# Kernel tuning notes

Hardware: AMD Instinct MI355X
Metric: run time of the kernel (lower is better)

The kernel has to match this reference:

```python
import jax, jax.numpy as jnp
import numpy as np
from jax import lax

# Constants matching PostProcess(conf_thres=0.4, iou_thres=0.5, merge=False, agnostic=False)
CONF_THRES = 0.4
IOU_THRES = 0.5
MAX_WH = 4096.0   # per-class box offset (agnostic=False)
MAX_DET = 300     # hardcoded in module
MAX_NMS = 30000   # cap on NMS candidates (yolov5 convention); JAX needs static shapes
B, N, NC = 16, 25200, 80


def setup_inputs() -> dict:
    key = jax.random.key(0)
    u = jax.random.uniform(key, (B, N, 5 + NC), dtype=jnp.float32)
    # cx,cy in [0,640); w,h in [2,102); obj and class scores in [0,1)
    scale = jnp.concatenate([jnp.array([640.0, 640.0, 100.0, 100.0], jnp.float32),
                             jnp.ones((1 + NC,), jnp.float32)])
    shift = jnp.concatenate([jnp.array([0.0, 0.0, 2.0, 2.0], jnp.float32),
                             jnp.zeros((1 + NC,), jnp.float32)])
    prediction = u * scale + shift
    return {"prediction": prediction}


def _cxcywh_to_xyxy(x):
    cx, cy, w, h = x[..., 0], x[..., 1], x[..., 2], x[..., 3]
    return jnp.stack([cx - 0.5 * w, cy - 0.5 * h, cx + 0.5 * w, cy + 0.5 * h], axis=-1)


def _process_one(x):  # x: [N, 5+NC]
    obj = x[:, 4]
    cls_conf = x[:, 5:] * obj[:, None]          # x[:,5:] *= x[:,4:5]
    box = _cxcywh_to_xyxy(x[:, :4])             # [N, 4]
    # multi-label candidate mask: obj > conf AND class conf > conf (x[xc] then x[:,5:] > conf)
    cand = (obj[:, None] > CONF_THRES) & (cls_conf > CONF_THRES)   # [N, NC]
    flat = jnp.where(cand, cls_conf, 0.0).reshape(-1)              # [N*NC]
    top_scores, top_idx = lax.top_k(flat, MAX_NMS)                 # static-size candidate set
    bi = top_idx // NC                                             # box index i
    cj = (top_idx % NC).astype(jnp.float32)                        # class index j
    cand_boxes = box[bi]                                           # [M, 4]
    scores0 = jnp.where(top_scores > CONF_THRES, top_scores, 0.0)  # 0 marks invalid/suppressed
    off_boxes = cand_boxes + cj[:, None] * MAX_WH                  # per-class offset for NMS
    areas = (off_boxes[:, 2] - off_boxes[:, 0]) * (off_boxes[:, 3] - off_boxes[:, 1])
    idx_range = jnp.arange(MAX_NMS)

    def step(scores, _):
        # greedy NMS: pick best remaining, suppress IoU > thresh (torchvision semantics)
        idx = jnp.argmax(scores)
        s = scores[idx]
        keep = s > 0.0
        b = off_boxes[idx]
        lt = jnp.maximum(b[:2], off_boxes[:, :2])
        rb = jnp.minimum(b[2:], off_boxes[:, 2:])
        wh = jnp.clip(rb - lt, 0.0)
        inter = wh[:, 0] * wh[:, 1]
        iou = inter / (areas[idx] + areas - inter + 1e-9)
        suppress = (iou > IOU_THRES) | (idx_range == idx)
        return jnp.where(suppress, 0.0, scores), (idx, keep)

    _, (keep_idx, keep_flag) = lax.scan(step, scores0, None, length=MAX_DET)
    rows = jnp.concatenate([cand_boxes[keep_idx],
                            top_scores[keep_idx][:, None],
                            cj[keep_idx][:, None]], axis=1)        # [MAX_DET, 6] = xyxy, conf, cls
    return jnp.where(keep_flag[:, None], rows, 0.0)


def reference(prediction):
    # Padded fixed-shape analogue of torch.stack(output): [B, MAX_DET, 6], zero rows = no detection
    return jax.vmap(_process_one)(prediction)
```

## Files before the change

kernel.cpp:

```cpp
#include <hip/hip_runtime.h>
#include <stdint.h>

#define BATCH 16
#define NROW 25200
#define NCLS 80
#define ROWF 85
#define MAXDET 300
#define MAXNMS 30000u
#define NBIN 3072
#define BASEBITS 0x3EC00000u
#define CAP 32768u
#define BATCH_FLOATS 2142000

#define PREBIN 2048
#define NBUCK 1024
#define CANDCAP 131072u
#define KMAX 2048u
#define TOPK 2048u
#define K2CAP 4096u

#define SORTCAP 1024
#define CH_SZ 128

#define TILE_ROWS 80
#define TILE_FLOATS 6800
#define RPB 400
#define SUBT 5
#define SBLK 63

#define ROWS_PER_BLK 256
#define SBLK2 99

__device__ __forceinline__ bool iou_gt_half(float ax1, float ay1, float ax2, float ay2, float aa,
                                            float bx1, float by1, float bx2, float by2, float ba) {
    float ltx = fmaxf(ax1, bx1), lty = fmaxf(ay1, by1);
    float rbx = fminf(ax2, bx2), rby = fminf(ay2, by2);
    float wx = fmaxf(__fsub_rn(rbx, ltx), 0.0f);
    float wy = fmaxf(__fsub_rn(rby, lty), 0.0f);
    float inter = __fmul_rn(wx, wy);
    float den = __fadd_rn(__fsub_rn(__fadd_rn(aa, ba), inter), 1e-9f);
    float t = __fmul_rn(0.5f, den);
    if (!(inter > t)) return false;
    float tg = __fmul_rn(0.50000012f, den);
    if (inter >= tg) return true;
    return __fdiv_rn(inter, den) > 0.5f;
}

__device__ __forceinline__ unsigned bin_of_bits(unsigned bits) {
    unsigned v = (bits - BASEBITS) >> 12;
    if (v > (unsigned)(NBIN - 1)) v = NBIN - 1;
    return v;
}

__global__ __launch_bounds__(256) void k_stage(const float* __restrict__ pred,
                                               unsigned* __restrict__ hist2,
                                               unsigned* __restrict__ ccnt,
                                               unsigned long long* __restrict__ cand,
                                               unsigned* __restrict__ oflow,
                                               int staged) {
    if (!staged) return;
    __shared__ unsigned shist[NBUCK];
    __shared__ unsigned long long skey[KMAX];
    __shared__ unsigned s_cnt, s_n, s_base;
    int bx = blockIdx.x;
    int b = bx / SBLK2, blk = bx - b * SBLK2;
    int t = threadIdx.x, lane = t & 63, wv = t >> 6;
    for (int i = t; i < NBUCK; i += 256) shist[i] = 0u;
    if (t == 0) s_cnt = 0u;
    __syncthreads();
    const float* pb = pred + (size_t)b * BATCH_FLOATS;
    int r0 = blk * ROWS_PER_BLK + wv * 64;
    int rown = NROW - r0;
    if (rown > 0) {
        if (rown > 64) rown = 64;
        float obj = 0.0f;
        if (lane < rown) obj = pb[(size_t)(r0 + lane) * ROWF + 4];
        unsigned long long live = __ballot(obj > 0.4f);
        while (live) {
            int j = (int)__builtin_ctzll(live);
            live &= live - 1ULL;
            float o = __shfl(obj, j);
            const float* rp = pb + (size_t)(r0 + j) * ROWF;
            unsigned grow = (unsigned)(r0 + j);
            {
                float s = __fmul_rn(rp[5 + lane], o);
                if (s >= 0.75f) {
                    unsigned bits = __float_as_uint(s);
                    unsigned bin = bin_of_bits(bits);
                    atomicAdd(&shist[bin - PREBIN], 1u);
                    unsigned u = atomicAdd(&s_cnt, 1u);
                    unsigned flat = grow * (unsigned)NCLS + (unsigned)lane;
                    if (u < KMAX)
                        skey[u] = ((unsigned long long)bits << 32) |
                                  (unsigned long long)(0xFFFFFFFFu - flat);
                    else oflow[b] = 1u;
                }
            }
            if (lane < 16) {
                int c = 64 + lane;
                float s = __fmul_rn(rp[5 + c], o);
                if (s >= 0.75f) {
                    unsigned bits = __float_as_uint(s);
                    unsigned bin = bin_of_bits(bits);
                    atomicAdd(&shist[bin - PREBIN], 1u);
                    unsigned u = atomicAdd(&s_cnt, 1u);
                    unsigned flat = grow * (unsigned)NCLS + (unsigned)c;
                    if (u < KMAX)
                        skey[u] = ((unsigned long long)bits << 32) |
                                  (unsigned long long)(0xFFFFFFFFu - flat);
                    else oflow[b] = 1u;
                }
            }
        }
    }
    __syncthreads();
    unsigned* gh = hist2 + (size_t)b * NBUCK;
    for (int i = t; i < NBUCK; i += 256) {
        unsigned v = shist[i];
        if (v) atomicAdd(&gh[i], v);
    }
    if (t == 0) {
        unsigned n = s_cnt;
        if (n > KMAX) n = KMAX;
        unsigned base = atomicAdd(&ccnt[b], n);
        if (base + n > CANDCAP) oflow[b] = 1u;
        s_n = n; s_base = base;
    }
    __syncthreads();
    unsigned n = s_n, base = s_base;
    if (base + n <= CANDCAP) {
        unsigned long long* cd = cand + (size_t)b * CANDCAP + base;
        for (unsigned k = t; k < n; k += 256) cd[k] = skey[k];
    }
}

__global__ __launch_bounds__(1024) void k_prep(const unsigned* __restrict__ hist2,
                                               const unsigned* __restrict__ ccnt,
                                               const unsigned* __restrict__ oflow,
                                               const unsigned long long* __restrict__ cand,
                                               unsigned* __restrict__ suf2,
                                               unsigned long long* __restrict__ keys2,
                                               int* __restrict__ meta,
                                               int staged) {
    __shared__ unsigned sS[NBUCK];
    __shared__ unsigned scur[NBUCK];
    __shared__ int s_cut, s_need, s_tot, s_T, s_valid;
    __shared__ unsigned s_bad, s_E;
    int b = blockIdx.x, t = threadIdx.x;
    unsigned h = hist2[(size_t)b * NBUCK + t];
    sS[t] = h;
    if (t == 0) { s_cut = -1; s_T = -1; s_bad = 0u; s_need = 0; s_tot = 0; s_E = 0u; }
    __syncthreads();
    if (h > (unsigned)SORTCAP) atomicOr(&s_bad, 1u);
    for (int off = 1; off < NBUCK; off <<= 1) {
        unsigned v = (t + off < NBUCK) ? sS[t + off] : 0u;
        __syncthreads();
        sS[t] += v;
        __syncthreads();
    }
    unsigned Sv = sS[t];
    unsigned Sn = (t + 1 < NBUCK) ? sS[t + 1] : 0u;
    if (Sv >= MAXNMS && Sn < MAXNMS) {
        s_cut = PREBIN + t; s_need = (int)(MAXNMS - Sn); s_tot = (int)Sv;
    }
    if (Sv >= TOPK && Sn < TOPK) { s_T = PREBIN + t; s_E = Sv; }
    unsigned* g2 = suf2 + (size_t)b * (NBUCK + 1);
    g2[t] = Sv;
    if (t == 0) g2[NBUCK] = 0u;
    scur[t] = Sn;
    __syncthreads();
    if (t == 0) {
        int valid = (staged && s_cut >= 0 && s_T >= 0 && s_bad == 0u &&
                     oflow[b] == 0u && ccnt[b] <= CANDCAP) ? 1 : 0;
        s_valid = valid;
        meta[b * 8 + 0] = valid ? s_cut : 0;
        meta[b * 8 + 1] = valid ? s_need : 0;
        meta[b * 8 + 2] = valid ? s_tot : 0;
        meta[b * 8 + 3] = valid;
        meta[b * 8 + 4] = valid ? s_T : 0;
        meta[b * 8 + 5] = valid ? (int)s_E : 0;
    }
    __syncthreads();
    if (s_valid) {
        int T = s_T;
        unsigned ccb = ccnt[b];
        const unsigned long long* cd = cand + (size_t)b * CANDCAP;
        unsigned long long* k2 = keys2 + (size_t)b * K2CAP;
        for (unsigned k = t; k < ccb; k += 1024) {
            unsigned long long key = cd[k];
            unsigned v = bin_of_bits((unsigned)(key >> 32));
            if ((int)v >= T) {
                unsigned pos = atomicAdd(&scur[v - PREBIN], 1u);
                if (pos < K2CAP) k2[pos] = key;
            }
        }
    }
}

__global__ __launch_bounds__(256) void k_hist_fb(const float* __restrict__ pred,
                                                 unsigned* __restrict__ hist,
                                                 const int* __restrict__ meta) {
    int bx = blockIdx.x;
    int b = bx / SBLK, blk = bx - b * SBLK;
    if (meta[b * 8 + 3]) return;
    __shared__ __align__(16) float rows[TILE_FLOATS];
    __shared__ unsigned shist[NBIN];
    int t = threadIdx.x, lane = t & 63, wv = t >> 6;
    for (int i = t; i < NBIN; i += 256) shist[i] = 0u;
    const float* pbase = pred + (size_t)b * BATCH_FLOATS + (size_t)blk * RPB * ROWF;
    for (int st = 0; st < SUBT; ++st) {
        __syncthreads();
        const float4* src = (const float4*)(pbase + (size_t)st * TILE_ROWS * ROWF);
        float4* dst = (float4*)rows;
        for (int i = t; i < TILE_FLOATS / 4; i += 256) dst[i] = src[i];
        __syncthreads();
        for (int r = wv; r < TILE_ROWS; r += 4) {
            float obj = rows[r * ROWF + 4];
            if (!(obj > 0.4f)) continue;
            for (int half = 0; half < 2; ++half) {
                int c = lane + (half << 6);
                if (c < NCLS) {
                    float s = __fmul_rn(rows[r * ROWF + 5 + c], obj);
                    if (s > 0.4f) atomicAdd(&shist[bin_of_bits(__float_as_uint(s))], 1u);
                }
            }
        }
    }
    __syncthreads();
    unsigned* gh = hist + (size_t)b * NBIN;
    for (int i = t; i < NBIN; i += 256) {
        unsigned v = shist[i];
        if (v) atomicAdd(&gh[i], v);
    }
}

__global__ __launch_bounds__(256) void k_scan_fb(const unsigned* __restrict__ hist,
                                                 unsigned* __restrict__ suf,
                                                 int* __restrict__ meta) {
    int b = blockIdx.x, t = threadIdx.x;
    if (meta[b * 8 + 3]) return;
    __shared__ unsigned sh[NBIN];
    __shared__ unsigned sS[NBIN];
    __shared__ unsigned cs[256];
    __shared__ int s_cut, s_need, s_tot;
    const unsigned* gh = hist + (size_t)b * NBIN;
    for (int i = t; i < NBIN; i += 256) sh[i] = gh[i];
    if (t == 0) { s_cut = 0; s_need = 0x7FFFFFFF; s_tot = 0; }
    __syncthreads();
    const int CHUNK = NBIN / 256;
    int base = t * CHUNK;
    unsigned tot = 0;
    for (int i = 0; i < CHUNK; ++i) tot += sh[base + i];
    cs[t] = tot;
    __syncthreads();
    for (int off = 1; off < 256; off <<= 1) {
        unsigned v = (t + off < 256) ? cs[t + off] : 0u;
        __syncthreads();
        cs[t] += v;
        __syncthreads();
    }
    unsigned after = (t + 1 < 256) ? cs[t + 1] : 0u;
    for (int i = CHUNK - 1; i >= 0; --i) {
        after += sh[base + i];
        sS[base + i] = after;
    }
    __syncthreads();
    unsigned* gs = suf + (size_t)b * (NBIN + 1);
    for (int i = t; i < NBIN; i += 256) gs[i] = sS[i];
    if (t == 0) gs[NBIN] = 0u;
    for (int i = 0; i < CHUNK; ++i) {
        int v = base + i;
        unsigned Sv = sS[v];
        unsigned Sn = (v + 1 < NBIN) ? sS[v + 1] : 0u;
        if (Sv >= MAXNMS && Sn < MAXNMS) {
            s_cut = v; s_need = (int)(MAXNMS - Sn); s_tot = (int)Sv;
        }
    }
    __syncthreads();
    if (t == 0) {
        int cut = s_cut, needv = s_need, totv = s_tot;
        if (sS[0] < MAXNMS) { cut = 0; needv = 0x7FFFFFFF; totv = (int)sS[0]; }
        meta[b * 8 + 0] = cut;
        meta[b * 8 + 1] = needv;
        meta[b * 8 + 2] = totv;
    }
}

__global__ __launch_bounds__(256) void k_scatter_fb(const float* __restrict__ pred,
                                                    const unsigned* __restrict__ suf,
                                                    const int* __restrict__ meta,
                                                    unsigned* __restrict__ cursor,
                                                    unsigned long long* __restrict__ keys) {
    int bx = blockIdx.x;
    int b = bx / SBLK, blk = bx - b * SBLK;
    if (meta[b * 8 + 3]) return;
    __shared__ __align__(16) float rows[TILE_FLOATS];
    int t = threadIdx.x, lane = t & 63, wv = t >> 6;
    int cutbin = meta[b * 8 + 0];
    const float* pbase = pred + (size_t)b * BATCH_FLOATS + (size_t)blk * RPB * ROWF;
    unsigned rowbase0 = (unsigned)(blk * RPB);
    const unsigned* gs = suf + (size_t)b * (NBIN + 1);
    unsigned* cur = cursor + (size_t)b * NBIN;
    unsigned long long* kb = keys + (size_t)b * CAP;
    for (int st = 0; st < SUBT; ++st) {
        __syncthreads();
        const float4* src = (const float4*)(pbase + (size_t)st * TILE_ROWS * ROWF);
        float4* dst = (float4*)rows;
        for (int i = t; i < TILE_FLOATS / 4; i += 256) dst[i] = src[i];
        __syncthreads();
        for (int r = wv; r < TILE_ROWS; r += 4) {
            float obj = rows[r * ROWF + 4];
            if (!(obj > 0.4f)) continue;
            unsigned grow = rowbase0 + (unsigned)(st * TILE_ROWS + r);
            for (int half = 0; half < 2; ++half) {
                int c = lane + (half << 6);
                if (c < NCLS) {
                    float s = __fmul_rn(rows[r * ROWF + 5 + c], obj);
                    if (s > 0.4f) {
                        unsigned bits = __float_as_uint(s);
                        unsigned bin = bin_of_bits(bits);
                        if ((int)bin >= cutbin) {
                            unsigned pos = gs[bin + 1] + atomicAdd(&cur[bin], 1u);
                            if (pos < CAP) {
                                unsigned flat = grow * (unsigned)NCLS + (unsigned)c;
                                kb[pos] = ((unsigned long long)bits << 32) |
                                          (unsigned long long)(0xFFFFFFFFu - flat);
                            }
                        }
                    }
                }
            }
        }
    }
}

__global__ __launch_bounds__(1024) void k_nms(const float* __restrict__ pred,
                                              const unsigned* __restrict__ suf,
                                              const unsigned* __restrict__ suf2,
                                              const int* __restrict__ meta,
                                              const unsigned* __restrict__ ccnt,
                                              const unsigned long long* __restrict__ keys,
                                              const unsigned long long* __restrict__ keys2,
                                              const unsigned long long* __restrict__ cand,
                                              float* __restrict__ out) {
    __shared__ unsigned sgsL[NBUCK + 1];
    __shared__ unsigned long long ktmp[SORTCAP];
    __shared__ unsigned long long skeys[SORTCAP];
    __shared__ unsigned maskW[CH_SZ][5];
    __shared__ unsigned sup0w[4];
    __shared__ float cbox[CH_SZ][9];
    __shared__ float kept[MAXDET][5];
    __shared__ int klist[MAXDET];
    __shared__ int s_nk, s_localk;
    __shared__ unsigned s_gc;

    int b = blockIdx.x;
    int tid = threadIdx.x;
    int lane = tid & 63, wv = tid >> 6;

    int cutbin = meta[b * 8 + 0];
    int needv  = meta[b * 8 + 1];
    unsigned total = (unsigned)meta[b * 8 + 2];
    int valid  = meta[b * 8 + 3];
    int Tbin   = meta[b * 8 + 4];
    unsigned E = valid ? (unsigned)meta[b * 8 + 5] : 0u;
    if (!valid && total > CAP) total = CAP;
    const unsigned* gs = suf + (size_t)b * (NBIN + 1);
    const unsigned* g2 = suf2 + (size_t)b * (NBUCK + 1);
    const unsigned long long* kb = keys + (size_t)b * CAP;
    const unsigned long long* k2 = keys2 + (size_t)b * K2CAP;
    const unsigned long long* cd = cand + (size_t)b * CANDCAP;
    unsigned ccb = valid ? ccnt[b] : 0u;
    if (ccb > CANDCAP) ccb = CANDCAP;
    const float* pb = pred + (size_t)b * BATCH_FLOATS;
    float* ob = out + (size_t)b * MAXDET * 6;

    if (valid) for (int i = tid; i < NBUCK + 1; i += 1024) sgsL[i] = g2[i];
    if (tid == 0) s_nk = 0;
    __syncthreads();

#define GSV(v) (valid ? sgsL[(v) - PREBIN] : gs[(v)])

    unsigned limit;
    if (needv == 0x7FFFFFFF) limit = total;
    else limit = GSV(cutbin + 1) + (unsigned)needv;
    if (limit > total) limit = total;

    unsigned p = 0;
    while (p < limit) {
        if (s_nk >= MAXDET) break;

        int lo = cutbin, hi = NBIN - 1, vs = NBIN - 1;
        while (lo <= hi) { int mid = (lo + hi) >> 1;
            if (GSV(mid) <= p + (unsigned)SORTCAP) { vs = mid; hi = mid - 1; } else lo = mid + 1; }
        unsigned gEnd = GSV(vs);
        bool phaseA = (!valid) || (p < E);
        if (valid && phaseA && gEnd > E) gEnd = E;
        if (gEnd > total) gEnd = total;
        if (gEnd <= p) { gEnd = p + (unsigned)SORTCAP; if (gEnd > total) gEnd = total; }
        unsigned G = gEnd - p;

        if (phaseA) {
            const unsigned long long* src = valid ? k2 : kb;
            unsigned myLo = 0, myHi = 0;
            unsigned long long raw = 0ULL;
            if (tid < (int)G) {
                unsigned idx = p + (unsigned)tid;
                int l2 = cutbin, h2 = NBIN - 1, v = cutbin;
                while (l2 <= h2) { int mid = (l2 + h2) >> 1;
                    if (GSV(mid) > idx) { v = mid; l2 = mid + 1; } else h2 = mid - 1; }
                unsigned bstart = GSV(v + 1);
                unsigned bend = GSV(v);
                raw = src[idx];
                myLo = (bstart > p) ? (bstart - p) : 0u;
                myHi = bend - p; if (myHi > G) myHi = G;
                ktmp[tid] = raw;
            }
            __syncthreads();
            if (tid < (int)G) {
                unsigned rank = 0;
                for (unsigned u = myLo; u < myHi; ++u) rank += (ktmp[u] > raw) ? 1u : 0u;
                skeys[myLo + rank] = raw;
            }
            __syncthreads();
        } else {
            int l0 = cutbin, h0 = NBIN - 1, w1 = cutbin;
            while (l0 <= h0) { int mid = (l0 + h0) >> 1;
                if (GSV(mid) > p) { w1 = mid; l0 = mid + 1; } else h0 = mid - 1; }
            if (tid == 0) s_gc = 0u;
            __syncthreads();
            for (unsigned k = tid; k < ccb; k += 1024) {
                unsigned long long key = cd[k];
                unsigned v = bin_of_bits((unsigned)(key >> 32));
                if ((int)v >= vs && (int)v <= w1) {
                    unsigned u = atomicAdd(&s_gc, 1u);
                    if (u < (unsigned)SORTCAP) ktmp[u] = key;
                }
            }
            __syncthreads();
            unsigned Gc = s_gc; if (Gc > (unsigned)SORTCAP) Gc = (unsigned)SORTCAP;
            if (tid < (int)Gc) {
                unsigned long long key = ktmp[tid];
                unsigned v = bin_of_bits((unsigned)(key >> 32));
                unsigned bstart = GSV(v + 1);
                unsigned rank = 0;
                for (unsigned u = 0; u < Gc; ++u) {
                    unsigned long long kk = ktmp[u];
                    unsigned vu = bin_of_bits((unsigned)(kk >> 32));
                    rank += (vu == v && kk > key) ? 1u : 0u;
                }
                skeys[(bstart - p) + rank] = key;
            }
            __syncthreads();
        }

        unsigned consumable = limit - p; if (consumable > G) consumable = G;

        for (unsigned c0 = 0; c0 < consumable; c0 += CH_SZ) {
            int nk0 = s_nk;
            if (nk0 >= MAXDET) break;
            int CH = (int)((consumable - c0 < (unsigned)CH_SZ) ? (consumable - c0) : (unsigned)CH_SZ);

            if (tid < CH_SZ * 5) maskW[tid / 5][tid % 5] = 0u;
            if (tid >= CH_SZ * 5 && tid < CH_SZ * 5 + 4) sup0w[tid - CH_SZ * 5] = 0u;
            if (tid < CH) {
                unsigned long long kk = skeys[c0 + tid];
                unsigned flat = 0xFFFFFFFFu - (unsigned)kk;
                unsigned bi = flat / (unsigned)NCLS;
                unsigned cc = flat - bi * (unsigned)NCLS;
                const float* rp = pb + (size_t)bi * ROWF;
                float cx = rp[0], cy = rp[1], wd = rp[2], ht = rp[3];
                float hw = __fmul_rn(0.5f, wd), hh = __fmul_rn(0.5f, ht);
                float off = __fmul_rn((float)cc, 4096.0f);
                float x1 = __fsub_rn(cx, hw), y1 = __fsub_rn(cy, hh);
                float x2 = __fadd_rn(cx, hw), y2 = __fadd_rn(cy, hh);
                float ox1 = __fadd_rn(x1, off), oy1 = __fadd_rn(y1, off);
                float ox2 = __fadd_rn(x2, off), oy2 = __fadd_rn(y2, off);
                cbox[tid][0] = ox1; cbox[tid][1] = oy1;
                cbox[tid][2] = ox2; cbox[tid][3] = oy2;
                cbox[tid][4] = __fmul_rn(__fsub_rn(ox2, ox1), __fsub_rn(oy2, oy1));
            }
            __syncthreads();

            {
                int col = tid & (CH_SZ - 1);
                int part = tid >> 7;
                if (col < CH) {
                    float bx1 = cbox[col][0], by1 = cbox[col][1];
                    float bx2 = cbox[col][2], by2 = cbox[col][3], ba = cbox[col][4];
                    unsigned part16 = 0u;
                    int rbase = part << 4;
                    for (int k = 0; k < 16; ++k) {
                        int i2 = rbase + k;
                        if (i2 >= col || i2 >= CH) break;
                        if (iou_gt_half(cbox[i2][0], cbox[i2][1], cbox[i2][2], cbox[i2][3],
                                        cbox[i2][4], bx1, by1, bx2, by2, ba))
                            part16 |= (1u << k);
                    }
                    if (part16)
                        atomicOr(&maskW[col][part >> 1], part16 << ((part & 1) << 4));
                    bool f = false;
                    for (int k2 = part; k2 < nk0; k2 += 8) {
                        if (iou_gt_half(kept[k2][0], kept[k2][1], kept[k2][2], kept[k2][3],
                                        kept[k2][4], bx1, by1, bx2, by2, ba)) f = true;
                    }
                    if (f) atomicOr(&sup0w[col >> 5], 1u << (col & 31));
                }
            }
            __syncthreads();

            if (wv == 0) {
                unsigned keptw = 0u;
                int nkv = nk0, lk = 0;
                unsigned pre0 = (lane < 4 && CH > 0) ? maskW[0][lane] : 0u;
                unsigned pre1 = (lane < 4 && CH > 1) ? maskW[1][lane] : 0u;
                for (int j = 0; j < CH && nkv < MAXDET; ++j) {
                    unsigned colw = pre0;
                    pre0 = pre1;
                    pre1 = (lane < 4 && (j + 2) < CH) ? maskW[j + 2][lane] : 0u;
                    bool hit = (keptw & colw) != 0u;
                    bool sup = __any(hit);
                    if ((sup0w[j >> 5] >> (j & 31)) & 1u) sup = true;
                    if (!sup) {
                        if (lane == (j >> 5)) keptw |= 1u << (j & 31);
                        if (lane == 0) klist[lk] = j;
                        lk++; nkv++;
                    }
                }
                if (lane == 0) { s_localk = lk; s_nk = nkv; }
            }
            __syncthreads();

            int lk = s_localk;
            for (int t2 = tid; t2 < lk; t2 += 1024) {
                int i = klist[t2];
                int oidx = nk0 + t2;
                kept[oidx][0] = cbox[i][0]; kept[oidx][1] = cbox[i][1];
                kept[oidx][2] = cbox[i][2]; kept[oidx][3] = cbox[i][3];
                kept[oidx][4] = cbox[i][4];
                unsigned long long kk = skeys[c0 + i];
                unsigned bits = (unsigned)(kk >> 32);
                unsigned flat = 0xFFFFFFFFu - (unsigned)kk;
                unsigned bi = flat / (unsigned)NCLS;
                unsigned cc = flat - bi * (unsigned)NCLS;
                const float* rp = pb + (size_t)bi * ROWF;
                float cx = rp[0], cy = rp[1], wd = rp[2], ht = rp[3];
                float hw = __fmul_rn(0.5f, wd), hh = __fmul_rn(0.5f, ht);
                float* orow = ob + (size_t)oidx * 6;
                orow[0] = __fsub_rn(cx, hw);
                orow[1] = __fsub_rn(cy, hh);
                orow[2] = __fadd_rn(cx, hw);
                orow[3] = __fadd_rn(cy, hh);
                orow[4] = __uint_as_float(bits);
                orow[5] = (float)cc;
            }
            __syncthreads();
        }
        p = gEnd;
    }
#undef GSV
}

extern "C" void kernel_launch(void* const* d_in, const int* in_sizes, int n_in,
                              void* d_out, int out_size, void* d_ws, size_t ws_size,
                              hipStream_t stream) {
    const float* pred = (const float*)d_in[0];
    float* outp = (float*)d_out;
    char* ws = (char*)d_ws;

    const size_t OFF_HIST  = 0;
    const size_t SZ_HIST   = (size_t)BATCH * NBIN * 4;
    const size_t OFF_CUR   = OFF_HIST + SZ_HIST;
    const size_t SZ_CUR    = (size_t)BATCH * NBIN * 4;
    const size_t OFF_H2    = OFF_CUR + SZ_CUR;
    const size_t SZ_H2     = (size_t)BATCH * NBUCK * 4;
    const size_t OFF_CCNT  = OFF_H2 + SZ_H2;
    const size_t SZ_CCNT   = (size_t)BATCH * 4;
    const size_t OFF_OFLW  = OFF_CCNT + SZ_CCNT;
    const size_t SZ_OFLW   = (size_t)BATCH * 4;
    const size_t OFF_META  = OFF_OFLW + SZ_OFLW;
    const size_t SZ_META   = (size_t)BATCH * 8 * 4;
    const size_t ZERO_SZ   = OFF_META + SZ_META;
    const size_t OFF_SUF   = ZERO_SZ;
    const size_t SZ_SUF    = (size_t)BATCH * (NBIN + 1) * 4;
    const size_t OFF_SUF2  = OFF_SUF + SZ_SUF;
    const size_t SZ_SUF2   = (size_t)BATCH * (NBUCK + 1) * 4;
    const size_t OFF_KEYS  = OFF_SUF2 + SZ_SUF2;
    const size_t SZ_KEYS   = (size_t)BATCH * CAP * 8;
    const size_t OFF_K2    = OFF_KEYS + SZ_KEYS;
    const size_t SZ_K2     = (size_t)BATCH * K2CAP * 8;
    const size_t OFF_CAND  = OFF_K2 + SZ_K2;
    const size_t SZ_CAND   = (size_t)BATCH * CANDCAP * 8;
    const size_t WS_NEEDED = OFF_CAND + SZ_CAND;

    int staged = (ws_size >= WS_NEEDED) ? 1 : 0;

    unsigned* hist             = (unsigned*)(ws + OFF_HIST);
    unsigned* cursor           = (unsigned*)(ws + OFF_CUR);
    unsigned* hist2            = (unsigned*)(ws + OFF_H2);
    unsigned* ccnt             = (unsigned*)(ws + OFF_CCNT);
    unsigned* oflow            = (unsigned*)(ws + OFF_OFLW);
    int* meta                  = (int*)(ws + OFF_META);
    unsigned* suf              = (unsigned*)(ws + OFF_SUF);
    unsigned* suf2             = (unsigned*)(ws + OFF_SUF2);
    unsigned long long* keys   = (unsigned long long*)(ws + OFF_KEYS);
    unsigned long long* keys2  = (unsigned long long*)(ws + OFF_K2);
    unsigned long long* cand   = (unsigned long long*)(ws + OFF_CAND);

    hipMemsetAsync(ws, 0, ZERO_SZ, stream);
    hipMemsetAsync(d_out, 0, (size_t)out_size * sizeof(float), stream);

    k_stage<<<dim3(BATCH * SBLK2), dim3(256), 0, stream>>>(pred, hist2, ccnt, cand, oflow, staged);
    k_prep<<<dim3(BATCH), dim3(1024), 0, stream>>>(hist2, ccnt, oflow, cand, suf2, keys2, meta, staged);
    k_hist_fb<<<dim3(BATCH * SBLK), dim3(256), 0, stream>>>(pred, hist, meta);
    k_scan_fb<<<dim3(BATCH), dim3(256), 0, stream>>>(hist, suf, meta);
    k_scatter_fb<<<dim3(BATCH * SBLK), dim3(256), 0, stream>>>(pred, suf, meta, cursor, keys);
    k_nms<<<dim3(BATCH), dim3(1024), 0, stream>>>(pred, suf, suf2, meta, ccnt, keys, keys2, cand, outp);
}
```

Before: 345.9 us.

## Stage prediction tiles through LDS with register prefetch in k_stage

The staging kernel no longer reads scattered per-row global memory inside a ballot loop. It now copies contiguous 80-row tiles into shared memory with coalesced float4 loads and prefetches the next tile into registers while the current one is processed. This makes global reads fully coalesced and overlaps load latency with compute. In exchange it reads all 85 columns of every row, including rows that fail the objectness filter, uses more LDS per block, and launches fewer blocks (63 per batch instead of 99).

```diff
diff --git a/kernel.cpp b/kernel.cpp
--- a/kernel.cpp
+++ b/kernel.cpp
@@ -24,12 +24,10 @@
 
 #define TILE_ROWS 80
 #define TILE_FLOATS 6800
+#define TILE_F4 1700
 #define RPB 400
 #define SUBT 5
 #define SBLK 63
-
-#define ROWS_PER_BLK 256
-#define SBLK2 99
 
 __device__ __forceinline__ bool iou_gt_half(float ax1, float ay1, float ax2, float ay2, float aa,
                                             float bx1, float by1, float bx2, float by2, float ba) {
@@ -59,35 +57,54 @@
                                                unsigned* __restrict__ oflow,
                                                int staged) {
     if (!staged) return;
+    __shared__ __align__(16) float rows[TILE_FLOATS];
     __shared__ unsigned shist[NBUCK];
     __shared__ unsigned long long skey[KMAX];
     __shared__ unsigned s_cnt, s_n, s_base;
     int bx = blockIdx.x;
-    int b = bx / SBLK2, blk = bx - b * SBLK2;
+    int b = bx / SBLK, blk = bx - b * SBLK;
     int t = threadIdx.x, lane = t & 63, wv = t >> 6;
     for (int i = t; i < NBUCK; i += 256) shist[i] = 0u;
     if (t == 0) s_cnt = 0u;
-    __syncthreads();
-    const float* pb = pred + (size_t)b * BATCH_FLOATS;
-    int r0 = blk * ROWS_PER_BLK + wv * 64;
-    int rown = NROW - r0;
-    if (rown > 0) {
-        if (rown > 64) rown = 64;
-        float obj = 0.0f;
-        if (lane < rown) obj = pb[(size_t)(r0 + lane) * ROWF + 4];
-        unsigned long long live = __ballot(obj > 0.4f);
-        while (live) {
-            int j = (int)__builtin_ctzll(live);
-            live &= live - 1ULL;
-            float o = __shfl(obj, j);
-            const float* rp = pb + (size_t)(r0 + j) * ROWF;
-            unsigned grow = (unsigned)(r0 + j);
+
+    const float* pbase = pred + (size_t)b * BATCH_FLOATS + (size_t)blk * RPB * ROWF;
+    int rowbase = blk * RPB;
+
+    float4 rg[7];
+    {
+        const float4* src = (const float4*)pbase;
+        #pragma unroll
+        for (int k = 0; k < 7; ++k) {
+            int idx = t + (k << 8);
+            if (idx < TILE_F4) rg[k] = src[idx];
+        }
+        float4* dst = (float4*)rows;
+        #pragma unroll
+        for (int k = 0; k < 7; ++k) {
+            int idx = t + (k << 8);
+            if (idx < TILE_F4) dst[idx] = rg[k];
+        }
+    }
+
+    for (int st = 0; st < SUBT; ++st) {
+        __syncthreads();
+        if (st + 1 < SUBT) {
+            const float4* src = (const float4*)(pbase + (size_t)(st + 1) * TILE_FLOATS);
+            #pragma unroll
+            for (int k = 0; k < 7; ++k) {
+                int idx = t + (k << 8);
+                if (idx < TILE_F4) rg[k] = src[idx];
+            }
+        }
+        for (int r = wv; r < TILE_ROWS; r += 4) {
+            float obj = rows[r * ROWF + 4];
+            if (!(obj > 0.4f)) continue;
+            unsigned grow = (unsigned)(rowbase + st * TILE_ROWS + r);
             {
-                float s = __fmul_rn(rp[5 + lane], o);
+                float s = __fmul_rn(rows[r * ROWF + 5 + lane], obj);
                 if (s >= 0.75f) {
                     unsigned bits = __float_as_uint(s);
-                    unsigned bin = bin_of_bits(bits);
-                    atomicAdd(&shist[bin - PREBIN], 1u);
+                    atomicAdd(&shist[bin_of_bits(bits) - PREBIN], 1u);
                     unsigned u = atomicAdd(&s_cnt, 1u);
                     unsigned flat = grow * (unsigned)NCLS + (unsigned)lane;
                     if (u < KMAX)
@@ -97,14 +114,12 @@
                 }
             }
             if (lane < 16) {
-                int c = 64 + lane;
-                float s = __fmul_rn(rp[5 + c], o);
+                float s = __fmul_rn(rows[r * ROWF + 69 + lane], obj);
                 if (s >= 0.75f) {
                     unsigned bits = __float_as_uint(s);
-                    unsigned bin = bin_of_bits(bits);
-                    atomicAdd(&shist[bin - PREBIN], 1u);
+                    atomicAdd(&shist[bin_of_bits(bits) - PREBIN], 1u);
                     unsigned u = atomicAdd(&s_cnt, 1u);
-                    unsigned flat = grow * (unsigned)NCLS + (unsigned)c;
+                    unsigned flat = grow * (unsigned)NCLS + (unsigned)(64 + lane);
                     if (u < KMAX)
                         skey[u] = ((unsigned long long)bits << 32) |
                                   (unsigned long long)(0xFFFFFFFFu - flat);
@@ -112,8 +127,17 @@
                 }
             }
         }
-    }
-    __syncthreads();
+        __syncthreads();
+        if (st + 1 < SUBT) {
+            float4* dst = (float4*)rows;
+            #pragma unroll
+            for (int k = 0; k < 7; ++k) {
+                int idx = t + (k << 8);
+                if (idx < TILE_F4) dst[idx] = rg[k];
+            }
+        }
+    }
+
     unsigned* gh = hist2 + (size_t)b * NBUCK;
     for (int i = t; i < NBUCK; i += 256) {
         unsigned v = shist[i];
@@ -610,7 +634,7 @@
     hipMemsetAsync(ws, 0, ZERO_SZ, stream);
     hipMemsetAsync(d_out, 0, (size_t)out_size * sizeof(float), stream);
 
-    k_stage<<<dim3(BATCH * SBLK2), dim3(256), 0, stream>>>(pred, hist2, ccnt, cand, oflow, staged);
+    k_stage<<<dim3(BATCH * SBLK), dim3(256), 0, stream>>>(pred, hist2, ccnt, cand, oflow, staged);
     k_prep<<<dim3(BATCH), dim3(1024), 0, stream>>>(hist2, ccnt, oflow, cand, suf2, keys2, meta, staged);
     k_hist_fb<<<dim3(BATCH * SBLK), dim3(256), 0, stream>>>(pred, hist, meta);
     k_scan_fb<<<dim3(BATCH), dim3(256), 0, stream>>>(hist, suf, meta);
```

After: 382.3 us. 1.1x slower.

## Stage prediction tiles into LDS with async global_load_lds double buffering

Applied to the files above, without the earlier changes.

The candidate-staging kernel now streams contiguous 48-row tiles of the prediction tensor into shared memory using the direct global-to-LDS load builtin, with two buffers so the next tile loads while the current one is scanned. Previously each wave read the objectness column with strided loads and then fetched class rows for live rows only. Blocks grow to 512 threads and cover 240 rows each. The kernel now reads the entire tensor contiguously instead of only live rows, trading more bytes moved for coalesced access. The per-block key capacity also shrinks, which makes the overflow path more likely.

```diff
diff --git a/kernel.cpp b/kernel.cpp
--- a/kernel.cpp
+++ b/kernel.cpp
@@ -15,7 +15,6 @@
 #define PREBIN 2048
 #define NBUCK 1024
 #define CANDCAP 131072u
-#define KMAX 2048u
 #define TOPK 2048u
 #define K2CAP 4096u
 
@@ -28,8 +27,15 @@
 #define SUBT 5
 #define SBLK 63
 
-#define ROWS_PER_BLK 256
-#define SBLK2 99
+#define SBLK_S 105
+#define RPB_S 240
+#define TROWS 48
+#define SUBT_S 5
+#define ST_F4 1020u
+#define B_F4 535500u
+#define BLK_F4 5100u
+#define TOTAL_F4 8568000u
+#define KMAXS 1536u
 
 __device__ __forceinline__ bool iou_gt_half(float ax1, float ay1, float ax2, float ay2, float aa,
                                             float bx1, float by1, float bx2, float by2, float ba) {
@@ -52,76 +58,97 @@
     return v;
 }
 
-__global__ __launch_bounds__(256) void k_stage(const float* __restrict__ pred,
+__device__ __forceinline__ void gload_lds16(const float4* g, float* lds_base_wave_uniform) {
+    __builtin_amdgcn_global_load_lds((const __attribute__((address_space(1))) void*)g,
+                                     (__attribute__((address_space(3))) void*)lds_base_wave_uniform,
+                                     16, 0, 0);
+}
+
+__device__ __forceinline__ void stage_tile(const float4* __restrict__ predf4,
+                                           float* lds_rows, unsigned tile_f4_base,
+                                           int wv, int lane) {
+    unsigned c0 = (unsigned)(wv << 7);
+    #pragma unroll
+    for (int j = 0; j < 2; ++j) {
+        unsigned cb = c0 + (unsigned)(j << 6);
+        unsigned gi = tile_f4_base + cb + (unsigned)lane;
+        if (gi > TOTAL_F4 - 1u) gi = TOTAL_F4 - 1u;
+        gload_lds16(predf4 + gi, lds_rows + (size_t)cb * 4);
+    }
+}
+
+__global__ __launch_bounds__(512) void k_stage(const float* __restrict__ pred,
                                                unsigned* __restrict__ hist2,
                                                unsigned* __restrict__ ccnt,
                                                unsigned long long* __restrict__ cand,
                                                unsigned* __restrict__ oflow,
                                                int staged) {
     if (!staged) return;
+    __shared__ __align__(16) float rows[2 * 4096];
     __shared__ unsigned shist[NBUCK];
-    __shared__ unsigned long long skey[KMAX];
+    __shared__ unsigned long long skey[KMAXS];
     __shared__ unsigned s_cnt, s_n, s_base;
     int bx = blockIdx.x;
-    int b = bx / SBLK2, blk = bx - b * SBLK2;
+    int b = bx / SBLK_S, blk = bx - b * SBLK_S;
     int t = threadIdx.x, lane = t & 63, wv = t >> 6;
-    for (int i = t; i < NBUCK; i += 256) shist[i] = 0u;
+    for (int i = t; i < NBUCK; i += 512) shist[i] = 0u;
     if (t == 0) s_cnt = 0u;
-    __syncthreads();
-    const float* pb = pred + (size_t)b * BATCH_FLOATS;
-    int r0 = blk * ROWS_PER_BLK + wv * 64;
-    int rown = NROW - r0;
-    if (rown > 0) {
-        if (rown > 64) rown = 64;
-        float obj = 0.0f;
-        if (lane < rown) obj = pb[(size_t)(r0 + lane) * ROWF + 4];
-        unsigned long long live = __ballot(obj > 0.4f);
-        while (live) {
-            int j = (int)__builtin_ctzll(live);
-            live &= live - 1ULL;
-            float o = __shfl(obj, j);
-            const float* rp = pb + (size_t)(r0 + j) * ROWF;
-            unsigned grow = (unsigned)(r0 + j);
+
+    const float4* predf4 = (const float4*)pred;
+    unsigned tb0 = (unsigned)b * B_F4 + (unsigned)blk * BLK_F4;
+    int rowbase = blk * RPB_S;
+
+    stage_tile(predf4, rows, tb0, wv, lane);
+    __syncthreads();
+
+    for (int st = 0; st < SUBT_S; ++st) {
+        int buf = st & 1;
+        if (st + 1 < SUBT_S)
+            stage_tile(predf4, rows + ((buf ^ 1) << 12), tb0 + (unsigned)(st + 1) * ST_F4, wv, lane);
+
+        const float* rb = rows + (buf << 12);
+        for (int r = wv; r < TROWS; r += 8) {
+            float obj = rb[r * ROWF + 4];
+            if (!(obj > 0.4f)) continue;
+            unsigned grow = (unsigned)(rowbase + st * TROWS + r);
             {
-                float s = __fmul_rn(rp[5 + lane], o);
+                float s = __fmul_rn(rb[r * ROWF + 5 + lane], obj);
                 if (s >= 0.75f) {
                     unsigned bits = __float_as_uint(s);
-                    unsigned bin = bin_of_bits(bits);
-                    atomicAdd(&shist[bin - PREBIN], 1u);
+                    atomicAdd(&shist[bin_of_bits(bits) - PREBIN], 1u);
                     unsigned u = atomicAdd(&s_cnt, 1u);
                     unsigned flat = grow * (unsigned)NCLS + (unsigned)lane;
-                    if (u < KMAX)
+                    if (u < KMAXS)
                         skey[u] = ((unsigned long long)bits << 32) |
                                   (unsigned long long)(0xFFFFFFFFu - flat);
                     else oflow[b] = 1u;
                 }
             }
             if (lane < 16) {
-                int c = 64 + lane;
-                float s = __fmul_rn(rp[5 + c], o);
+                float s = __fmul_rn(rb[r * ROWF + 69 + lane], obj);
                 if (s >= 0.75f) {
                     unsigned bits = __float_as_uint(s);
-                    unsigned bin = bin_of_bits(bits);
-                    atomicAdd(&shist[bin - PREBIN], 1u);
+                    atomicAdd(&shist[bin_of_bits(bits) - PREBIN], 1u);
                     unsigned u = atomicAdd(&s_cnt, 1u);
-                    unsigned flat = grow * (unsigned)NCLS + (unsigned)c;
-                    if (u < KMAX)
+                    unsigned flat = grow * (unsigned)NCLS + (unsigned)(64 + lane);
+                    if (u < KMAXS)
                         skey[u] = ((unsigned long long)bits << 32) |
                                   (unsigned long long)(0xFFFFFFFFu - flat);
                     else oflow[b] = 1u;
                 }
             }
         }
-    }
-    __syncthreads();
+        __syncthreads();
+    }
+
     unsigned* gh = hist2 + (size_t)b * NBUCK;
-    for (int i = t; i < NBUCK; i += 256) {
+    for (int i = t; i < NBUCK; i += 512) {
         unsigned v = shist[i];
         if (v) atomicAdd(&gh[i], v);
     }
     if (t == 0) {
         unsigned n = s_cnt;
-        if (n > KMAX) n = KMAX;
+        if (n > KMAXS) n = KMAXS;
         unsigned base = atomicAdd(&ccnt[b], n);
         if (base + n > CANDCAP) oflow[b] = 1u;
         s_n = n; s_base = base;
@@ -130,7 +157,7 @@
     unsigned n = s_n, base = s_base;
     if (base + n <= CANDCAP) {
         unsigned long long* cd = cand + (size_t)b * CANDCAP + base;
-        for (unsigned k = t; k < n; k += 256) cd[k] = skey[k];
+        for (unsigned k = t; k < n; k += 512) cd[k] = skey[k];
     }
 }
 
@@ -610,7 +637,7 @@
     hipMemsetAsync(ws, 0, ZERO_SZ, stream);
     hipMemsetAsync(d_out, 0, (size_t)out_size * sizeof(float), stream);
 
-    k_stage<<<dim3(BATCH * SBLK2), dim3(256), 0, stream>>>(pred, hist2, ccnt, cand, oflow, staged);
+    k_stage<<<dim3(BATCH * SBLK_S), dim3(512), 0, stream>>>(pred, hist2, ccnt, cand, oflow, staged);
     k_prep<<<dim3(BATCH), dim3(1024), 0, stream>>>(hist2, ccnt, oflow, cand, suf2, keys2, meta, staged);
     k_hist_fb<<<dim3(BATCH * SBLK), dim3(256), 0, stream>>>(pred, hist, meta);
     k_scan_fb<<<dim3(BATCH), dim3(256), 0, stream>>>(hist, suf, meta);
```

Result: faster. 321.5 us (-7.1%).
